# Kernel optimization log

Hardware: AMD Instinct MI355X
Metric: run time of the kernel (lower is better)

Reference implementation:

```python
import jax, jax.numpy as jnp
import numpy as np
from jax import ops as jops

N_NODES = 100000
N_EDGES = 1600000
NEG_SLOPE = 0.2
LN_EPS = 1e-5


def setup_inputs() -> dict:
    key = jax.random.key(0)
    ks = jax.random.split(key, 12)
    inp = {
        "x": jax.random.normal(ks[0], (N_NODES, 4), jnp.float32),
        "edge_index": jax.random.randint(ks[1], (2, N_EDGES), 0, N_NODES, jnp.int64 if jax.config.jax_enable_x64 else jnp.int32),
        # layer 1: GATv2Conv(4, 16, heads=4)
        "W1l": jax.random.normal(ks[2], (4, 64), jnp.float32) * 0.5,
        "W1r": jax.random.normal(ks[3], (4, 64), jnp.float32) * 0.5,
        "a1": jax.random.normal(ks[4], (4, 16), jnp.float32) * 0.5,  # [heads, out]
        "b1": jax.random.normal(ks[5], (64,), jnp.float32) * 0.1,
        "g1": jnp.ones((64,), jnp.float32),
        "be1": jnp.zeros((64,), jnp.float32),
        # layer 2: GATv2Conv(64, 32, heads=1)
        "W2l": jax.random.normal(ks[6], (64, 32), jnp.float32) * 0.125,
        "W2r": jax.random.normal(ks[7], (64, 32), jnp.float32) * 0.125,
        "a2": jax.random.normal(ks[8], (1, 32), jnp.float32) * 0.5,
        "b2": jax.random.normal(ks[9], (32,), jnp.float32) * 0.1,
        "g2": jnp.ones((32,), jnp.float32),
        "be2": jnp.zeros((32,), jnp.float32),
    }
    return inp


def _add_self_loops(edge_index, n):
    loop = jnp.arange(n, dtype=edge_index.dtype)
    return jnp.concatenate([edge_index, jnp.stack([loop, loop])], axis=1)


def _gatv2(x, src, dst, Wl, Wr, att, bias, heads, out_ch, n):
    # x: [N, F]; Wl/Wr: [F, heads*out_ch]; att: [heads, out_ch]
    xl = (x @ Wl).reshape(n, heads, out_ch)  # source transform
    xr = (x @ Wr).reshape(n, heads, out_ch)  # target transform
    e = xl[src] + xr[dst]                     # [E, H, C]
    e = jnp.where(e >= 0, e, NEG_SLOPE * e)   # LeakyReLU(0.2)
    logits = jnp.einsum('ehc,hc->eh', e, att)  # [E, H]
    # segment softmax over destination node
    m = jops.segment_max(logits, dst, num_segments=n)  # [N, H]
    ex = jnp.exp(logits - m[dst])
    denom = jops.segment_sum(ex, dst, num_segments=n)  # [N, H]
    alpha = ex / denom[dst]                            # [E, H]
    out = jops.segment_sum(alpha[:, :, None] * xl[src], dst, num_segments=n)  # [N, H, C]
    return out.reshape(n, heads * out_ch) + bias


def _layernorm(x, g, b):
    mu = jnp.mean(x, axis=-1, keepdims=True)
    var = jnp.mean(jnp.square(x - mu), axis=-1, keepdims=True)
    return (x - mu) * jax.lax.rsqrt(var + LN_EPS) * g + b


def reference(x, edge_index, W1l, W1r, a1, b1, g1, be1, W2l, W2r, a2, b2, g2, be2):
    n = x.shape[0]
    ei = _add_self_loops(edge_index, n)
    src, dst = ei[0], ei[1]
    h = _gatv2(x, src, dst, W1l, W1r, a1, b1, heads=4, out_ch=16, n=n)
    h = _layernorm(h, g1, be1)
    h = jnp.where(h > 0, h, jnp.expm1(h))  # ELU
    h = _gatv2(h, src, dst, W2l, W2r, a2, b2, heads=1, out_ch=32, n=n)
    h = _layernorm(h, g2, be2)
    return h
```

## Files before the change

kernel.cpp:

```cpp
#include <hip/hip_runtime.h>
#include <math.h>

#define NN 100000
#define E0 1600000
#define ETOT (E0 + NN)
#define NEG 0.2f

#define NB 512
#define BS 196
#define CHUNK 4096
#define PPT 16
#define MAXP 4096

__device__ __forceinline__ float leaky(float v) { return fmaxf(v, NEG * v); }

__global__ void k_bhist(const int* __restrict__ ei, int* __restrict__ bcnt) {
    __shared__ int h[NB];
    int tid = threadIdx.x;
    for (int i = tid; i < NB; i += 256) h[i] = 0;
    __syncthreads();
    int stride = gridDim.x * 256;
    for (int e = blockIdx.x * 256 + tid; e < E0; e += stride)
        atomicAdd(&h[ei[E0 + e] / BS], 1);
    __syncthreads();
    for (int i = tid; i < NB; i += 256)
        if (h[i]) atomicAdd(&bcnt[i], h[i]);
}

__global__ void k_bscan(const int* __restrict__ bcnt, int* __restrict__ boff,
                        int* __restrict__ srcsBase, int* __restrict__ cursor) {
    __shared__ int s[NB];
    int tid = threadIdx.x;
    int v = bcnt[tid];
    s[tid] = v;
    __syncthreads();
    for (int off = 1; off < NB; off <<= 1) {
        int t = (tid >= off) ? s[tid - off] : 0;
        __syncthreads();
        s[tid] += t;
        __syncthreads();
    }
    int excl = s[tid] - v;
    boff[tid] = excl;
    cursor[tid] = excl;
    int n0 = tid * BS;
    if (n0 > NN) n0 = NN;
    srcsBase[tid] = excl + n0;
}

__global__ void k_bin(const int* __restrict__ ei, int* __restrict__ cursor,
                      int2* __restrict__ binned) {
    __shared__ int hist[NB];
    __shared__ int basesh[NB];
    int tid = threadIdx.x;
    long long cbase = (long long)blockIdx.x * CHUNK;
    for (int i = tid; i < NB; i += 256) hist[i] = 0;
    __syncthreads();
    int srcv[PPT], dstv[PPT], rank[PPT], bkt[PPT];
#pragma unroll
    for (int k = 0; k < PPT; ++k) {
        long long e = cbase + k * 256 + tid;
        if (e < E0) {
            int s_ = ei[e];
            int d_ = ei[E0 + e];
            int b = d_ / BS;
            rank[k] = atomicAdd(&hist[b], 1);
            srcv[k] = s_;
            dstv[k] = d_;
            bkt[k] = b;
        } else {
            bkt[k] = -1;
        }
    }
    __syncthreads();
    for (int i = tid; i < NB; i += 256)
        if (hist[i] > 0) basesh[i] = atomicAdd(&cursor[i], hist[i]);
    __syncthreads();
#pragma unroll
    for (int k = 0; k < PPT; ++k)
        if (bkt[k] >= 0) {
            int2 p;
            p.x = srcv[k];
            p.y = dstv[k];
            binned[basesh[bkt[k]] + rank[k]] = p;
        }
}

__global__ void k_bfin(const int2* __restrict__ binned, const int* __restrict__ bcnt,
                       const int* __restrict__ boff, const int* __restrict__ srcsBase,
                       int* __restrict__ rs, int* __restrict__ srcs) {
    int b = blockIdx.x;
    int n0 = b * BS;
    if (n0 >= NN) return;
    int nd = NN - n0;
    if (nd > BS) nd = BS;
    int cnt = bcnt[b];
    if (cnt > MAXP) cnt = MAXP;
    int base = boff[b];
    int sb = srcsBase[b];
    __shared__ int ldsCnt[256];
    __shared__ int scanA[256];
    __shared__ int rowOffE[256];
    __shared__ int stage[MAXP + BS];
    int tid = threadIdx.x;
    ldsCnt[tid] = 0;
    __syncthreads();
    int srcv[PPT], dl_[PPT], rk_[PPT];
#pragma unroll
    for (int k = 0; k < PPT; ++k) {
        int i = k * 256 + tid;
        if (i < cnt) {
            int2 p = binned[base + i];
            int dl = p.y - n0;
            rk_[k] = atomicAdd(&ldsCnt[dl], 1);
            srcv[k] = p.x;
            dl_[k] = dl;
        } else {
            dl_[k] = -1;
        }
    }
    __syncthreads();
    int v = (tid < nd) ? ldsCnt[tid] + 1 : 0;
    scanA[tid] = v;
    __syncthreads();
    for (int off = 1; off < 256; off <<= 1) {
        int t = (tid >= off) ? scanA[tid - off] : 0;
        __syncthreads();
        scanA[tid] += t;
        __syncthreads();
    }
    rowOffE[tid] = scanA[tid] - v;
    __syncthreads();
    if (tid < nd) {
        int e = rowOffE[tid];
        rs[n0 + tid] = sb + e;
        stage[e] = n0 + tid;
    }
    __syncthreads();
#pragma unroll
    for (int k = 0; k < PPT; ++k)
        if (dl_[k] >= 0) stage[rowOffE[dl_[k]] + 1 + rk_[k]] = srcv[k];
    __syncthreads();
    int tot = cnt + nd;
    for (int i = tid; i < tot; i += 256) srcs[sb + i] = stage[i];
}

__global__ void k_gat1(const float* __restrict__ x, const float* __restrict__ Wl,
                       const float* __restrict__ Wr, const float* __restrict__ att,
                       const int* __restrict__ rs, const int* __restrict__ srcs,
                       const float* __restrict__ b, const float* __restrict__ g,
                       const float* __restrict__ be, float* __restrict__ h) {
    int n = blockIdx.x * (blockDim.x >> 6) + (threadIdx.x >> 6);
    if (n >= NN) return;
    int lane = threadIdx.x & 63;
    float wl0 = Wl[lane], wl1 = Wl[64 + lane], wl2 = Wl[128 + lane],
          wl3 = Wl[192 + lane];
    const float4 xd = *(const float4*)(x + n * 4);
    float xrd = xd.x * Wr[lane] + xd.y * Wr[64 + lane] + xd.z * Wr[128 + lane] +
                xd.w * Wr[192 + lane];
    float attl = att[lane];
    int beg = rs[n];
    int end = (n == NN - 1) ? ETOT : rs[n + 1];
    float acc = 0.f, den = 0.f;
    int base = beg;
    while (base < end) {
        int cnt = end - base;
        if (cnt > 64) cnt = 64;
        int si = (lane < cnt) ? srcs[base + lane] : 0;
        int j = 0;
        for (; j + 2 <= cnt; j += 2) {
            int s0 = __builtin_amdgcn_readlane(si, j);
            int s1 = __builtin_amdgcn_readlane(si, j + 1);
            const float4 xa = *(const float4*)(x + s0 * 4);
            const float4 xb = *(const float4*)(x + s1 * 4);
            float xlsa = xa.x * wl0 + xa.y * wl1 + xa.z * wl2 + xa.w * wl3;
            float xlsb = xb.x * wl0 + xb.y * wl1 + xb.z * wl2 + xb.w * wl3;
            float ta = leaky(xlsa + xrd) * attl;
            float tb = leaky(xlsb + xrd) * attl;
            ta += __shfl_xor(ta, 1); tb += __shfl_xor(tb, 1);
            ta += __shfl_xor(ta, 2); tb += __shfl_xor(tb, 2);
            ta += __shfl_xor(ta, 4); tb += __shfl_xor(tb, 4);
            ta += __shfl_xor(ta, 8); tb += __shfl_xor(tb, 8);
            float exa = __expf(ta), exb = __expf(tb);
            acc += exa * xlsa;
            acc += exb * xlsb;
            den += exa + exb;
        }
        if (j < cnt) {
            int s0 = __builtin_amdgcn_readlane(si, j);
            const float4 xa = *(const float4*)(x + s0 * 4);
            float xlsa = xa.x * wl0 + xa.y * wl1 + xa.z * wl2 + xa.w * wl3;
            float ta = leaky(xlsa + xrd) * attl;
            ta += __shfl_xor(ta, 1);
            ta += __shfl_xor(ta, 2);
            ta += __shfl_xor(ta, 4);
            ta += __shfl_xor(ta, 8);
            float exa = __expf(ta);
            acc += exa * xlsa;
            den += exa;
        }
        base += cnt;
    }
    float v = acc / den + b[lane];
    float s1 = v;
#pragma unroll
    for (int m = 1; m < 64; m <<= 1) s1 += __shfl_xor(s1, m);
    float mu = s1 * (1.f / 64.f);
    float c = v - mu;
    float sq = c * c;
#pragma unroll
    for (int m = 1; m < 64; m <<= 1) sq += __shfl_xor(sq, m);
    float y = c * rsqrtf(sq * (1.f / 64.f) + 1e-5f) * g[lane] + be[lane];
    h[(long long)n * 64 + lane] = y > 0.f ? y : expm1f(y);
}

__global__ void k_lin2(const float* __restrict__ h, const float* __restrict__ Wl,
                       const float* __restrict__ Wr, float* __restrict__ xl2,
                       float* __restrict__ xr2) {
    __shared__ float wl_s[2048];
    __shared__ float wr_s[2048];
    for (int i = threadIdx.x; i < 2048; i += blockDim.x) {
        wl_s[i] = Wl[i];
        wr_s[i] = Wr[i];
    }
    __syncthreads();
    int t = blockIdx.x * blockDim.x + threadIdx.x;
    if (t >= NN * 32) return;
    int n = t >> 5, j = t & 31;
    const float* hr = h + (long long)n * 64;
    float al = 0.f, ar = 0.f;
#pragma unroll 8
    for (int k = 0; k < 64; ++k) {
        float hv = hr[k];
        al += hv * wl_s[k * 32 + j];
        ar += hv * wr_s[k * 32 + j];
    }
    xl2[(long long)n * 32 + j] = al;
    xr2[(long long)n * 32 + j] = ar;
}

__global__ void k_gat2(const float* __restrict__ xl2, const float* __restrict__ xr2,
                       const float* __restrict__ att, const int* __restrict__ rs,
                       const int* __restrict__ srcs, const float* __restrict__ b,
                       const float* __restrict__ g, const float* __restrict__ be,
                       float* __restrict__ out) {
    int n = blockIdx.x * (blockDim.x >> 6) + (threadIdx.x >> 6);
    if (n >= NN) return;
    int lane = threadIdx.x & 63;
    int half = lane >> 5, c = lane & 31;
    float xrd = xr2[(long long)n * 32 + c];
    float attl = att[c];
    int beg = rs[n];
    int end = (n == NN - 1) ? ETOT : rs[n + 1];
    float acc = 0.f, den = 0.f;
    int base = beg;
    while (base < end) {
        int cnt = end - base;
        if (cnt > 64) cnt = 64;
        int si = (lane < cnt) ? srcs[base + lane] : 0;
        int nit = (cnt + 1) >> 1;
        int j = 0;
        for (; j + 2 <= nit; j += 2) {
            int i0 = j * 2 + half, i1 = (j + 1) * 2 + half;
            bool v0 = i0 < cnt, v1 = i1 < cnt;
            int s0 = __shfl(si, v0 ? i0 : 0);
            int s1 = __shfl(si, v1 ? i1 : 0);
            float xlsa = xl2[(long long)s0 * 32 + c];
            float xlsb = xl2[(long long)s1 * 32 + c];
            float ta = leaky(xlsa + xrd) * attl;
            float tb = leaky(xlsb + xrd) * attl;
            ta += __shfl_xor(ta, 1);  tb += __shfl_xor(tb, 1);
            ta += __shfl_xor(ta, 2);  tb += __shfl_xor(tb, 2);
            ta += __shfl_xor(ta, 4);  tb += __shfl_xor(tb, 4);
            ta += __shfl_xor(ta, 8);  tb += __shfl_xor(tb, 8);
            ta += __shfl_xor(ta, 16); tb += __shfl_xor(tb, 16);
            float exa = v0 ? __expf(ta) : 0.f;
            float exb = v1 ? __expf(tb) : 0.f;
            acc += exa * xlsa;
            acc += exb * xlsb;
            den += exa + exb;
        }
        if (j < nit) {
            int i0 = j * 2 + half;
            bool v0 = i0 < cnt;
            int s0 = __shfl(si, v0 ? i0 : 0);
            float xlsa = xl2[(long long)s0 * 32 + c];
            float ta = leaky(xlsa + xrd) * attl;
            ta += __shfl_xor(ta, 1);
            ta += __shfl_xor(ta, 2);
            ta += __shfl_xor(ta, 4);
            ta += __shfl_xor(ta, 8);
            ta += __shfl_xor(ta, 16);
            float exa = v0 ? __expf(ta) : 0.f;
            acc += exa * xlsa;
            den += exa;
        }
        base += cnt;
    }
    acc += __shfl_xor(acc, 32);
    den += __shfl_xor(den, 32);
    float v = acc / den + b[c];
    float s1 = v;
#pragma unroll
    for (int m = 1; m < 32; m <<= 1) s1 += __shfl_xor(s1, m);
    float mu = s1 * (1.f / 32.f);
    float cc = v - mu;
    float sq = cc * cc;
#pragma unroll
    for (int m = 1; m < 32; m <<= 1) sq += __shfl_xor(sq, m);
    float y = cc * rsqrtf(sq * (1.f / 32.f) + 1e-5f) * g[c] + be[c];
    if (half == 0) out[(long long)n * 32 + c] = y;
}

extern "C" void kernel_launch(void* const* d_in, const int* in_sizes, int n_in,
                              void* d_out, int out_size, void* d_ws, size_t ws_size,
                              hipStream_t stream) {
    const float* x   = (const float*)d_in[0];
    const int*   ei  = (const int*)d_in[1];
    const float* W1l = (const float*)d_in[2];
    const float* W1r = (const float*)d_in[3];
    const float* a1  = (const float*)d_in[4];
    const float* b1  = (const float*)d_in[5];
    const float* g1  = (const float*)d_in[6];
    const float* be1 = (const float*)d_in[7];
    const float* W2l = (const float*)d_in[8];
    const float* W2r = (const float*)d_in[9];
    const float* a2  = (const float*)d_in[10];
    const float* b2  = (const float*)d_in[11];
    const float* g2  = (const float*)d_in[12];
    const float* be2 = (const float*)d_in[13];
    float* out = (float*)d_out;

    float* ws = (float*)d_ws;
    float* h   = ws;
    float* xl2 = ws + 6400000;
    float* xr2 = ws + 9600000;
    int2* binned = (int2*)ws;
    int* ib        = (int*)(ws + 12800000);
    int* rs        = ib;
    int* srcs      = ib + 100000;
    int* bcnt      = ib + 1800000;
    int* boff      = ib + 1800000 + NB;
    int* srcsBase  = ib + 1800000 + 2 * NB;
    int* cursor    = ib + 1800000 + 3 * NB;

    hipMemsetAsync(bcnt, 0, NB * sizeof(int), stream);
    k_bhist<<<256, 256, 0, stream>>>(ei, bcnt);
    k_bscan<<<1, NB, 0, stream>>>(bcnt, boff, srcsBase, cursor);
    k_bin<<<(E0 + CHUNK - 1) / CHUNK, 256, 0, stream>>>(ei, cursor, binned);
    k_bfin<<<NB, 256, 0, stream>>>(binned, bcnt, boff, srcsBase, rs, srcs);

    k_gat1<<<(NN + 3) / 4, 256, 0, stream>>>(x, W1l, W1r, a1, rs, srcs,
                                             b1, g1, be1, h);
    k_lin2<<<(NN * 32 + 255) / 256, 256, 0, stream>>>(h, W2l, W2r, xl2, xr2);
    k_gat2<<<(NN + 3) / 4, 256, 0, stream>>>(xl2, xr2, a2, rs, srcs,
                                             b2, g2, be2, out);
}
```

Measured before the change: 260.4 us.

## Process 8 edges per wave iteration in GAT kernels with per-lane channel slices

Both GAT aggregation kernels are restructured so each wave handles 8 edges at once, with 8 lanes per edge each covering a slice of channels (8 for layer 1, 4 for layer 2). Per-edge logit reductions shrink to 1–3 shuffles, and partial accumulators are combined across edge groups with xor-shuffles after the loop. The kernels become grid-stride loops over nodes with fixed grid sizes, and layer-1 weights are held in registers. The aim is to raise memory-level parallelism on the gathers and cut per-edge shuffle overhead, at the cost of higher register pressure and wasted lanes on nodes with few edges.

```diff
diff --git a/kernel.cpp b/kernel.cpp
--- a/kernel.cpp
+++ b/kernel.cpp
@@ -150,68 +150,77 @@
                        const int* __restrict__ rs, const int* __restrict__ srcs,
                        const float* __restrict__ b, const float* __restrict__ g,
                        const float* __restrict__ be, float* __restrict__ h) {
-    int n = blockIdx.x * (blockDim.x >> 6) + (threadIdx.x >> 6);
-    if (n >= NN) return;
     int lane = threadIdx.x & 63;
-    float wl0 = Wl[lane], wl1 = Wl[64 + lane], wl2 = Wl[128 + lane],
-          wl3 = Wl[192 + lane];
-    const float4 xd = *(const float4*)(x + n * 4);
-    float xrd = xd.x * Wr[lane] + xd.y * Wr[64 + lane] + xd.z * Wr[128 + lane] +
-                xd.w * Wr[192 + lane];
-    float attl = att[lane];
-    int beg = rs[n];
-    int end = (n == NN - 1) ? ETOT : rs[n + 1];
-    float acc = 0.f, den = 0.f;
-    int base = beg;
-    while (base < end) {
-        int cnt = end - base;
-        if (cnt > 64) cnt = 64;
-        int si = (lane < cnt) ? srcs[base + lane] : 0;
-        int j = 0;
-        for (; j + 2 <= cnt; j += 2) {
-            int s0 = __builtin_amdgcn_readlane(si, j);
-            int s1 = __builtin_amdgcn_readlane(si, j + 1);
-            const float4 xa = *(const float4*)(x + s0 * 4);
-            const float4 xb = *(const float4*)(x + s1 * 4);
-            float xlsa = xa.x * wl0 + xa.y * wl1 + xa.z * wl2 + xa.w * wl3;
-            float xlsb = xb.x * wl0 + xb.y * wl1 + xb.z * wl2 + xb.w * wl3;
-            float ta = leaky(xlsa + xrd) * attl;
-            float tb = leaky(xlsb + xrd) * attl;
-            ta += __shfl_xor(ta, 1); tb += __shfl_xor(tb, 1);
-            ta += __shfl_xor(ta, 2); tb += __shfl_xor(tb, 2);
-            ta += __shfl_xor(ta, 4); tb += __shfl_xor(tb, 4);
-            ta += __shfl_xor(ta, 8); tb += __shfl_xor(tb, 8);
-            float exa = __expf(ta), exb = __expf(tb);
-            acc += exa * xlsa;
-            acc += exb * xlsb;
-            den += exa + exb;
-        }
-        if (j < cnt) {
-            int s0 = __builtin_amdgcn_readlane(si, j);
-            const float4 xa = *(const float4*)(x + s0 * 4);
-            float xlsa = xa.x * wl0 + xa.y * wl1 + xa.z * wl2 + xa.w * wl3;
-            float ta = leaky(xlsa + xrd) * attl;
-            ta += __shfl_xor(ta, 1);
-            ta += __shfl_xor(ta, 2);
-            ta += __shfl_xor(ta, 4);
-            ta += __shfl_xor(ta, 8);
-            float exa = __expf(ta);
-            acc += exa * xlsa;
-            den += exa;
-        }
-        base += cnt;
-    }
-    float v = acc / den + b[lane];
-    float s1 = v;
-#pragma unroll
-    for (int m = 1; m < 64; m <<= 1) s1 += __shfl_xor(s1, m);
-    float mu = s1 * (1.f / 64.f);
-    float c = v - mu;
-    float sq = c * c;
-#pragma unroll
-    for (int m = 1; m < 64; m <<= 1) sq += __shfl_xor(sq, m);
-    float y = c * rsqrtf(sq * (1.f / 64.f) + 1e-5f) * g[lane] + be[lane];
-    h[(long long)n * 64 + lane] = y > 0.f ? y : expm1f(y);
+    int wave = (blockIdx.x * blockDim.x + threadIdx.x) >> 6;
+    int nwaves = (gridDim.x * blockDim.x) >> 6;
+    int e_i = lane >> 3;
+    int sub = lane & 7;
+    float wl[4][8], wr[4][8], at[8];
+#pragma unroll
+    for (int k = 0; k < 4; ++k)
+#pragma unroll
+        for (int j = 0; j < 8; ++j) {
+            wl[k][j] = Wl[k * 64 + sub * 8 + j];
+            wr[k][j] = Wr[k * 64 + sub * 8 + j];
+        }
+#pragma unroll
+    for (int j = 0; j < 8; ++j) at[j] = att[sub * 8 + j];
+
+    for (int n = wave; n < NN; n += nwaves) {
+        const float4 xd = *(const float4*)(x + (long long)n * 4);
+        float xrd[8];
+#pragma unroll
+        for (int j = 0; j < 8; ++j)
+            xrd[j] = xd.x * wr[0][j] + xd.y * wr[1][j] + xd.z * wr[2][j] +
+                     xd.w * wr[3][j];
+        int beg = rs[n];
+        int end = (n == NN - 1) ? ETOT : rs[n + 1];
+        float acc[8] = {0.f, 0.f, 0.f, 0.f, 0.f, 0.f, 0.f, 0.f};
+        float den = 0.f;
+        for (int base = beg; base < end; base += 8) {
+            int slot = base + e_i;
+            bool valid = slot < end;
+            int s = srcs[valid ? slot : beg];
+            const float4 xa = *(const float4*)(x + (long long)s * 4);
+            float xls[8];
+            float p = 0.f;
+#pragma unroll
+            for (int j = 0; j < 8; ++j) {
+                float t = xa.x * wl[0][j] + xa.y * wl[1][j] + xa.z * wl[2][j] +
+                          xa.w * wl[3][j];
+                xls[j] = t;
+                float u = t + xrd[j];
+                u = fmaxf(u, NEG * u);
+                p += u * at[j];
+            }
+            p += __shfl_xor(p, 1);
+            float ex = valid ? __expf(p) : 0.f;
+            den += ex;
+#pragma unroll
+            for (int j = 0; j < 8; ++j) acc[j] += ex * xls[j];
+        }
+#pragma unroll
+        for (int m = 8; m <= 32; m <<= 1) {
+#pragma unroll
+            for (int j = 0; j < 8; ++j) acc[j] += __shfl_xor(acc[j], m);
+            den += __shfl_xor(den, m);
+        }
+        float v = acc[0];
+#pragma unroll
+        for (int j = 1; j < 8; ++j) v = (e_i == j) ? acc[j] : v;
+        int cf = sub * 8 + e_i;
+        v = v / den + b[cf];
+        float s1 = v;
+#pragma unroll
+        for (int m = 1; m < 64; m <<= 1) s1 += __shfl_xor(s1, m);
+        float mu = s1 * (1.f / 64.f);
+        float c = v - mu;
+        float sq = c * c;
+#pragma unroll
+        for (int m = 1; m < 64; m <<= 1) sq += __shfl_xor(sq, m);
+        float y = c * rsqrtf(sq * (1.f / 64.f) + 1e-5f) * g[cf] + be[cf];
+        h[(long long)n * 64 + cf] = y > 0.f ? y : expm1f(y);
+    }
 }
 
 __global__ void k_lin2(const float* __restrict__ h, const float* __restrict__ Wl,
@@ -244,72 +253,66 @@
                        const int* __restrict__ srcs, const float* __restrict__ b,
                        const float* __restrict__ g, const float* __restrict__ be,
                        float* __restrict__ out) {
-    int n = blockIdx.x * (blockDim.x >> 6) + (threadIdx.x >> 6);
-    if (n >= NN) return;
     int lane = threadIdx.x & 63;
-    int half = lane >> 5, c = lane & 31;
-    float xrd = xr2[(long long)n * 32 + c];
-    float attl = att[c];
-    int beg = rs[n];
-    int end = (n == NN - 1) ? ETOT : rs[n + 1];
-    float acc = 0.f, den = 0.f;
-    int base = beg;
-    while (base < end) {
-        int cnt = end - base;
-        if (cnt > 64) cnt = 64;
-        int si = (lane < cnt) ? srcs[base + lane] : 0;
-        int nit = (cnt + 1) >> 1;
-        int j = 0;
-        for (; j + 2 <= nit; j += 2) {
-            int i0 = j * 2 + half, i1 = (j + 1) * 2 + half;
-            bool v0 = i0 < cnt, v1 = i1 < cnt;
-            int s0 = __shfl(si, v0 ? i0 : 0);
-            int s1 = __shfl(si, v1 ? i1 : 0);
-            float xlsa = xl2[(long long)s0 * 32 + c];
-            float xlsb = xl2[(long long)s1 * 32 + c];
-            float ta = leaky(xlsa + xrd) * attl;
-            float tb = leaky(xlsb + xrd) * attl;
-            ta += __shfl_xor(ta, 1);  tb += __shfl_xor(tb, 1);
-            ta += __shfl_xor(ta, 2);  tb += __shfl_xor(tb, 2);
-            ta += __shfl_xor(ta, 4);  tb += __shfl_xor(tb, 4);
-            ta += __shfl_xor(ta, 8);  tb += __shfl_xor(tb, 8);
-            ta += __shfl_xor(ta, 16); tb += __shfl_xor(tb, 16);
-            float exa = v0 ? __expf(ta) : 0.f;
-            float exb = v1 ? __expf(tb) : 0.f;
-            acc += exa * xlsa;
-            acc += exb * xlsb;
-            den += exa + exb;
-        }
-        if (j < nit) {
-            int i0 = j * 2 + half;
-            bool v0 = i0 < cnt;
-            int s0 = __shfl(si, v0 ? i0 : 0);
-            float xlsa = xl2[(long long)s0 * 32 + c];
-            float ta = leaky(xlsa + xrd) * attl;
-            ta += __shfl_xor(ta, 1);
-            ta += __shfl_xor(ta, 2);
-            ta += __shfl_xor(ta, 4);
-            ta += __shfl_xor(ta, 8);
-            ta += __shfl_xor(ta, 16);
-            float exa = v0 ? __expf(ta) : 0.f;
-            acc += exa * xlsa;
-            den += exa;
-        }
-        base += cnt;
-    }
-    acc += __shfl_xor(acc, 32);
-    den += __shfl_xor(den, 32);
-    float v = acc / den + b[c];
-    float s1 = v;
-#pragma unroll
-    for (int m = 1; m < 32; m <<= 1) s1 += __shfl_xor(s1, m);
-    float mu = s1 * (1.f / 32.f);
-    float cc = v - mu;
-    float sq = cc * cc;
-#pragma unroll
-    for (int m = 1; m < 32; m <<= 1) sq += __shfl_xor(sq, m);
-    float y = cc * rsqrtf(sq * (1.f / 32.f) + 1e-5f) * g[c] + be[c];
-    if (half == 0) out[(long long)n * 32 + c] = y;
+    int wave = (blockIdx.x * blockDim.x + threadIdx.x) >> 6;
+    int nwaves = (gridDim.x * blockDim.x) >> 6;
+    int e_i = lane >> 3;
+    int cg = lane & 7;
+    float at[4];
+#pragma unroll
+    for (int j = 0; j < 4; ++j) at[j] = att[cg * 4 + j];
+
+    for (int n = wave; n < NN; n += nwaves) {
+        const float4 xr4 = *(const float4*)(xr2 + (long long)n * 32 + cg * 4);
+        float xrd[4] = {xr4.x, xr4.y, xr4.z, xr4.w};
+        int beg = rs[n];
+        int end = (n == NN - 1) ? ETOT : rs[n + 1];
+        float acc[4] = {0.f, 0.f, 0.f, 0.f};
+        float den = 0.f;
+        for (int base = beg; base < end; base += 8) {
+            int slot = base + e_i;
+            bool valid = slot < end;
+            int s = srcs[valid ? slot : beg];
+            const float4 xa = *(const float4*)(xl2 + (long long)s * 32 + cg * 4);
+            float xls[4] = {xa.x, xa.y, xa.z, xa.w};
+            float p = 0.f;
+#pragma unroll
+            for (int j = 0; j < 4; ++j) {
+                float u = xls[j] + xrd[j];
+                u = fmaxf(u, NEG * u);
+                p += u * at[j];
+            }
+            p += __shfl_xor(p, 1);
+            p += __shfl_xor(p, 2);
+            p += __shfl_xor(p, 4);
+            float ex = valid ? __expf(p) : 0.f;
+            den += ex;
+#pragma unroll
+            for (int j = 0; j < 4; ++j) acc[j] += ex * xls[j];
+        }
+#pragma unroll
+        for (int m = 8; m <= 32; m <<= 1) {
+#pragma unroll
+            for (int j = 0; j < 4; ++j) acc[j] += __shfl_xor(acc[j], m);
+            den += __shfl_xor(den, m);
+        }
+        int e3 = e_i & 3;
+        float v = acc[0];
+#pragma unroll
+        for (int j = 1; j < 4; ++j) v = (e3 == j) ? acc[j] : v;
+        int cf = cg * 4 + e3;
+        v = v / den + b[cf];
+        float s1 = v;
+#pragma unroll
+        for (int m = 1; m < 64; m <<= 1) s1 += __shfl_xor(s1, m);
+        float mu = s1 * (1.f / 64.f);
+        float cc = v - mu;
+        float sq = cc * cc;
+#pragma unroll
+        for (int m = 1; m < 64; m <<= 1) sq += __shfl_xor(sq, m);
+        float y = cc * rsqrtf(sq * (1.f / 64.f) + 1e-5f) * g[cf] + be[cf];
+        if (e_i < 4) out[(long long)n * 32 + cf] = y;
+    }
 }
 
 extern "C" void kernel_launch(void* const* d_in, const int* in_sizes, int n_in,
@@ -350,9 +353,7 @@
     k_bin<<<(E0 + CHUNK - 1) / CHUNK, 256, 0, stream>>>(ei, cursor, binned);
     k_bfin<<<NB, 256, 0, stream>>>(binned, bcnt, boff, srcsBase, rs, srcs);
 
-    k_gat1<<<(NN + 3) / 4, 256, 0, stream>>>(x, W1l, W1r, a1, rs, srcs,
-                                             b1, g1, be1, h);
+    k_gat1<<<1024, 256, 0, stream>>>(x, W1l, W1r, a1, rs, srcs, b1, g1, be1, h);
     k_lin2<<<(NN * 32 + 255) / 256, 256, 0, stream>>>(h, W2l, W2r, xl2, xr2);
-    k_gat2<<<(NN + 3) / 4, 256, 0, stream>>>(xl2, xr2, a2, rs, srcs,
-                                             b2, g2, be2, out);
-}
+    k_gat2<<<2048, 256, 0, stream>>>(xl2, xr2, a2, rs, srcs, b2, g2, be2, out);
+}
```

Result: faster. 228.7 us (-12.2%).
